# Performance work log

Measured on AMD Instinct MI355X. Metric: run time of the kernel, lower is better.

The kernel has to match this reference:

```python
import jax, jax.numpy as jnp
import numpy as np

B, L, D, H, PD = 1, 512, 1024, 16, 128
HW = D // H  # 64


def _layernorm(x, g, b, eps=1e-5):
    mu = jnp.mean(x, axis=-1, keepdims=True)
    var = jnp.var(x, axis=-1, keepdims=True)
    return (x - mu) * jax.lax.rsqrt(var + eps) * g + b


def setup_inputs() -> dict:
    key = jax.random.key(0)
    ks = jax.random.split(key, 16)
    s = 0.02
    return {
        "sequence_state": jax.random.normal(ks[0], (B, L, D), jnp.float32),
        "pairwise_state": jax.random.normal(ks[1], (B, L, L, PD), jnp.float32),
        "mask": jnp.ones((B, L), dtype=bool),
        # layernorm before attention
        "ln1_g": jnp.ones((D,), jnp.float32),
        "ln1_b": jnp.zeros((D,), jnp.float32),
        # attention params (weights stored [in, out])
        "proj_w": jax.random.normal(ks[2], (D, 3 * H * HW), jnp.float32) * s,
        "g_w": jax.random.normal(ks[3], (D, H * HW), jnp.float32) * s,
        "g_b": jnp.ones((H * HW,), jnp.float32),
        "o_w": jax.random.normal(ks[4], (H * HW, D), jnp.float32) * s,
        "o_b": jnp.zeros((D,), jnp.float32),
        # pair-to-sequence bias
        "p2s_ln_g": jnp.ones((PD,), jnp.float32),
        "p2s_ln_b": jnp.zeros((PD,), jnp.float32),
        "p2s_w": jax.random.normal(ks[5], (PD, H), jnp.float32) * s,
        # residue MLP
        "mlp_ln_g": jnp.ones((D,), jnp.float32),
        "mlp_ln_b": jnp.zeros((D,), jnp.float32),
        "mlp_w1": jax.random.normal(ks[6], (D, 4 * D), jnp.float32) * s,
        "mlp_b1": jnp.zeros((4 * D,), jnp.float32),
        "mlp_w2": jax.random.normal(ks[7], (4 * D, D), jnp.float32) * s,
        "mlp_b2": jnp.zeros((D,), jnp.float32),
    }


def reference(sequence_state, pairwise_state, mask,
              ln1_g, ln1_b, proj_w, g_w, g_b, o_w, o_b,
              p2s_ln_g, p2s_ln_b, p2s_w,
              mlp_ln_g, mlp_ln_b, mlp_w1, mlp_b1, mlp_w2, mlp_b2):
    # PairToSequence: LN over pairwise feature dim, then project to per-head bias
    z = _layernorm(pairwise_state, p2s_ln_g, p2s_ln_b)
    bias = jnp.einsum("bqkp,ph->bhqk", z, p2s_w)  # [B,H,L,L]

    # Pre-attention layernorm
    y = _layernorm(sequence_state, ln1_g, ln1_b)

    # Gated attention with pairwise bias
    t = (y @ proj_w).reshape(B, L, H, 3 * HW)
    q, k, v = jnp.split(t, 3, axis=-1)  # each [B,L,H,HW]
    q = q * (HW ** -0.5)
    a = jnp.einsum("bqhc,bkhc->bhqk", q, k) + bias
    a = jnp.where(mask[:, None, None, :], a, -jnp.inf)
    a = jax.nn.softmax(a, axis=-1)
    o = jnp.einsum("bhqk,bkhc->bqhc", a, v).reshape(B, L, H * HW)
    gate = jax.nn.sigmoid(y @ g_w + g_b)
    o = (gate * o) @ o_w + o_b

    # residual (dropout=0 -> identity)
    s = sequence_state + o

    # ResidueMLP: x + Linear(ReLU(Linear(LN(x))))
    h = _layernorm(s, mlp_ln_g, mlp_ln_b)
    h = jax.nn.relu(h @ mlp_w1 + mlp_b1) @ mlp_w2 + mlp_b2
    return s + h
```

## Files before the change

### kernel.cpp

```cpp
#include <hip/hip_runtime.h>


typedef __attribute__((ext_vector_type(8))) short bfrag;
typedef __attribute__((ext_vector_type(4))) float f32x4;
typedef unsigned short ushort_t;
typedef unsigned int u32;

#define AS1 __attribute__((address_space(1)))
#define AS3 __attribute__((address_space(3)))

__device__ __forceinline__ void gll16(const void* g, void* l) {
  __builtin_amdgcn_global_load_lds((const AS1 u32*)g, (AS3 u32*)l, 16, 0, 0);
}

__device__ __forceinline__ unsigned short f2b(float x) {
  union { float f; unsigned u; } a; a.f = x;
  unsigned r = a.u + 0x7fffu + ((a.u >> 16) & 1u);
  return (unsigned short)(r >> 16);
}
__device__ __forceinline__ unsigned pack2(float a, float b) {
  return (unsigned)f2b(a) | ((unsigned)f2b(b) << 16);
}

#define OFF_GW    ((size_t)0)
#define OFF_SB    ((size_t)65536)
#define OFF_P     (OFF_SB   + (size_t)16777216)
#define OFF_Y     (OFF_P    + (size_t)8388608)
#define OFF_QS    (OFF_Y    + (size_t)1048576)
#define OFF_KS    (OFF_QS   + (size_t)1048576)
#define OFF_VT    (OFF_KS   + (size_t)1048576)
#define OFF_GATE  (OFF_VT   + (size_t)1048576)
#define OFF_OG    (OFF_GATE + (size_t)2097152)
#define OFF_S     (OFF_OG   + (size_t)1048576)
#define OFF_HLN   (OFF_S    + (size_t)2097152)
#define OFF_H1    (OFF_HLN  + (size_t)1048576)
#define OFF_PART  (OFF_H1   + (size_t)4194304)
#define OFF_WPG   (OFF_PART + (size_t)8388608)
#define OFF_WO    (OFF_WPG  + (size_t)8388608)
#define OFF_W1    (OFF_WO   + (size_t)2097152)
#define OFF_W2    (OFF_W1   + (size_t)8388608)

__global__ __launch_bounds__(256) void p2s_setup(
    const float* __restrict__ g, const float* __restrict__ b,
    const float* __restrict__ w, float* __restrict__ gw) {
  int t = threadIdx.x;
  for (int i = t; i < 2048; i += 256) {
    int h = i >> 7, f = i & 127;
    gw[h * 128 + f] = g[f] * w[f * 16 + h];
  }
  if (t < 16) {
    float a = 0.f, c = 0.f;
    for (int f = 0; f < 128; f++) { a += g[f] * w[f * 16 + t]; c += b[f] * w[f * 16 + t]; }
    gw[2048 + t] = a;
    gw[2064 + t] = c;
  }
}

__global__ __launch_bounds__(256) void p2s_main(
    const float* __restrict__ pw, const float* __restrict__ gw,
    float* __restrict__ biasOut) {
  __shared__ float xs[16 * 132];
  __shared__ float gwt[16 * 132];
  const int t = threadIdx.x;
  const long pair0 = (long)blockIdx.x * 16;
  const int p = t >> 4;
  const int h = t & 15;
  const int f0 = h * 8;

  float4 w0 = *(const float4*)&gw[p * 128 + f0];
  float4 w1 = *(const float4*)&gw[p * 128 + f0 + 4];
  *(float4*)&gwt[p * 132 + f0]     = w0;
  *(float4*)&gwt[p * 132 + f0 + 4] = w1;
  const float* src = pw + pair0 * 128 + (long)t * 8;
  float4 x0 = *(const float4*)src;
  float4 x1 = *(const float4*)(src + 4);
  *(float4*)&xs[p * 132 + f0]     = x0;
  *(float4*)&xs[p * 132 + f0 + 4] = x1;

  float s  = x0.x + x0.y + x0.z + x0.w + x1.x + x1.y + x1.z + x1.w;
  float sq = x0.x*x0.x + x0.y*x0.y + x0.z*x0.z + x0.w*x0.w
           + x1.x*x1.x + x1.y*x1.y + x1.z*x1.z + x1.w*x1.w;
#pragma unroll
  for (int m = 1; m < 16; m <<= 1) { s += __shfl_xor(s, m); sq += __shfl_xor(sq, m); }
  float mu  = s * (1.f / 128.f);
  float var = sq * (1.f / 128.f) - mu * mu;
  float rs  = rsqrtf(var + 1e-5f);

  __syncthreads();

  float acc = 0.f;
#pragma unroll 8
  for (int f = 0; f < 128; f += 4) {
    float4 xv = *(const float4*)&xs[p * 132 + f];
    float4 wv = *(const float4*)&gwt[h * 132 + f];
    acc += xv.x * wv.x + xv.y * wv.y + xv.z * wv.z + xv.w * wv.w;
  }
  float c1 = gw[2048 + h], c2 = gw[2064 + h];
  biasOut[(long)h * 262144 + pair0 + p] = rs * (acc - mu * c1) + c2;
}

__device__ __forceinline__ void transp_tile(
    const float* __restrict__ W, ushort_t* __restrict__ Wt, int K, int N,
    int bx, int by, int tid) {
  __shared__ float tile[64][65];
  int n0 = bx * 64, k0 = by * 64;
  int tr = tid >> 4, tc = (tid & 15) * 4;
#pragma unroll
  for (int i = 0; i < 4; i++) {
    int r = tr + i * 16;
    float4 v = *(const float4*)&W[(long)(k0 + r) * N + n0 + tc];
    tile[r][tc] = v.x; tile[r][tc + 1] = v.y; tile[r][tc + 2] = v.z; tile[r][tc + 3] = v.w;
  }
  __syncthreads();
  int nr = tid >> 2, kk = (tid & 3) * 16;
  ushort_t* dst = Wt + (long)(n0 + nr) * K + k0 + kk;
  uint4 q;
  q.x = pack2(tile[kk + 0][nr], tile[kk + 1][nr]);
  q.y = pack2(tile[kk + 2][nr], tile[kk + 3][nr]);
  q.z = pack2(tile[kk + 4][nr], tile[kk + 5][nr]);
  q.w = pack2(tile[kk + 6][nr], tile[kk + 7][nr]);
  *(uint4*)dst = q;
  uint4 q2;
  q2.x = pack2(tile[kk + 8][nr],  tile[kk + 9][nr]);
  q2.y = pack2(tile[kk + 10][nr], tile[kk + 11][nr]);
  q2.z = pack2(tile[kk + 12][nr], tile[kk + 13][nr]);
  q2.w = pack2(tile[kk + 14][nr], tile[kk + 15][nr]);
  *(uint4*)(dst + 8) = q2;
}

__global__ __launch_bounds__(256) void transpose_all(
    const float* __restrict__ proj_w, const float* __restrict__ g_w,
    const float* __restrict__ o_w, const float* __restrict__ w1,
    const float* __restrict__ w2,
    ushort_t* __restrict__ wpg, ushort_t* __restrict__ wo,
    ushort_t* __restrict__ w1t, ushort_t* __restrict__ w2t) {
  int id = blockIdx.x, tid = threadIdx.x;
  if (id < 768)       transp_tile(proj_w, wpg, 1024, 3072, id % 48, id / 48, tid);
  else if (id < 1024) { int j = id - 768;  transp_tile(g_w, wpg + (long)3072 * 1024, 1024, 1024, j % 16, j / 16, tid); }
  else if (id < 1280) { int j = id - 1024; transp_tile(o_w, wo, 1024, 1024, j % 16, j / 16, tid); }
  else if (id < 2304) { int j = id - 1280; transp_tile(w1, w1t, 1024, 4096, j % 64, j / 64, tid); }
  else                { int j = id - 2304; transp_tile(w2, w2t, 4096, 1024, j % 16, j / 16, tid); }
}

__global__ __launch_bounds__(256) void ln_rows(
    const float* __restrict__ x, const float* __restrict__ g,
    const float* __restrict__ b, ushort_t* __restrict__ out) {
  __shared__ float ps[8];
  int row = blockIdx.x, t = threadIdx.x;
  float4 v = *(const float4*)(x + (long)row * 1024 + t * 4);
  float s  = v.x + v.y + v.z + v.w;
  float sq = v.x*v.x + v.y*v.y + v.z*v.z + v.w*v.w;
#pragma unroll
  for (int k = 1; k < 64; k <<= 1) { s += __shfl_xor(s, k); sq += __shfl_xor(sq, k); }
  if ((t & 63) == 0) { ps[t >> 6] = s; ps[4 + (t >> 6)] = sq; }
  __syncthreads();
  s  = ps[0] + ps[1] + ps[2] + ps[3];
  sq = ps[4] + ps[5] + ps[6] + ps[7];
  float mu = s * (1.f / 1024.f);
  float rs = rsqrtf(sq * (1.f / 1024.f) - mu * mu + 1e-5f);
  float4 gv = *(const float4*)(g + t * 4);
  float4 bv = *(const float4*)(b + t * 4);
  uint2 o;
  o.x = pack2((v.x - mu) * rs * gv.x + bv.x, (v.y - mu) * rs * gv.y + bv.y);
  o.y = pack2((v.z - mu) * rs * gv.z + bv.z, (v.w - mu) * rs * gv.w + bv.w);
  *(uint2*)(out + (long)row * 1024 + t * 4) = o;
}

template <int EPI>
__global__ __launch_bounds__(256) void gemm128(
    const ushort_t* __restrict__ A, const ushort_t* __restrict__ Bt,
    int lda, int ldb, int Ksplit,
    const float* __restrict__ bias1,
    float* __restrict__ outF, ushort_t* __restrict__ outH, int ldc,
    ushort_t* __restrict__ qs, ushort_t* __restrict__ ks,
    ushort_t* __restrict__ vt, float* __restrict__ gatebuf) {
  __shared__ ushort_t As[64 * 32];
  __shared__ ushort_t Bs[128 * 32];
  const int tid = threadIdx.x;
  const int w = tid >> 6, lane = tid & 63;
  const int ln = lane & 15, quad = lane >> 4;
  const int wm = w >> 1, wn = w & 1;
  const int m0 = blockIdx.y * 64, n0 = blockIdx.x * 128;
  const int z = blockIdx.z;
  const int Koff = (EPI == 0) ? z * Ksplit : 0;

  const ushort_t* ga  = A  + (long)(m0 + (tid >> 2)) * lda + Koff + (tid & 3) * 8;
  const ushort_t* gb0 = Bt + (long)(n0 + (tid >> 2)) * ldb + Koff + (tid & 3) * 8;
  const ushort_t* gb1 = gb0 + (long)64 * ldb;
  unsigned wofs = __builtin_amdgcn_readfirstlane(w * 1024);
  char* lA  = (char*)As + wofs;
  char* lB0 = (char*)Bs + wofs;
  char* lB1 = (char*)Bs + 4096 + wofs;

  f32x4 acc[2][4];
#pragma unroll
  for (int i = 0; i < 2; i++)
#pragma unroll
    for (int j = 0; j < 4; j++) acc[i][j] = (f32x4){0.f, 0.f, 0.f, 0.f};

  for (int k0 = 0; k0 < Ksplit; k0 += 32) {
    gll16(ga + k0, lA);
    gll16(gb0 + k0, lB0);
    gll16(gb1 + k0, lB1);
    __syncthreads();
    bfrag a0 = *(const bfrag*)&As[(wm * 32 + ln) * 32 + quad * 8];
    bfrag a1 = *(const bfrag*)&As[(wm * 32 + 16 + ln) * 32 + quad * 8];
#pragma unroll
    for (int bn = 0; bn < 4; bn++) {
      bfrag b = *(const bfrag*)&Bs[(wn * 64 + bn * 16 + ln) * 32 + quad * 8];
      acc[0][bn] = __builtin_amdgcn_mfma_f32_16x16x32_bf16(a0, b, acc[0][bn], 0, 0, 0);
      acc[1][bn] = __builtin_amdgcn_mfma_f32_16x16x32_bf16(a1, b, acc[1][bn], 0, 0, 0);
    }
    __syncthreads();
  }

#pragma unroll
  for (int am = 0; am < 2; am++) {
#pragma unroll
    for (int bn = 0; bn < 4; bn++) {
      int ocol = n0 + wn * 64 + bn * 16 + ln;
#pragma unroll
      for (int r = 0; r < 4; r++) {
        int orow = m0 + wm * 32 + am * 16 + quad * 4 + r;
        float v = acc[am][bn][r];
        if (EPI == 0) {
          outF[(long)z * 524288 + (long)orow * ldc + ocol] = v;
        } else if (EPI == 3) {
          v = fmaxf(v + bias1[ocol], 0.f);
          outH[(long)orow * ldc + ocol] = f2b(v);
        } else if (EPI == 6) {
          if (ocol < 3072) {
            int h = ocol / 192, j = ocol - h * 192;
            if (j < 64)       qs[((long)h * 512 + orow) * 64 + j] = f2b(v * 0.125f);
            else if (j < 128) ks[((long)h * 512 + orow) * 64 + (j - 64)] = f2b(v);
            else              vt[((long)h * 64 + (j - 128)) * 512 + orow] = f2b(v);
          } else {
            int gcol = ocol - 3072;
            float gv = v + bias1[gcol];
            gatebuf[(long)orow * 1024 + gcol] = 1.f / (1.f + __expf(-gv));
          }
        }
      }
    }
  }
}

template <int EPI>
__global__ __launch_bounds__(256) void gemm_bt(
    const ushort_t* __restrict__ A, const ushort_t* __restrict__ Bt,
    const float* __restrict__ bias2, int ldb2,
    float* __restrict__ outF, ushort_t* __restrict__ outH,
    int K, int ldc, long sAz, long sBz, long sCz, long sB2z) {
  __shared__ ushort_t As[64 * 40];
  __shared__ ushort_t Bs[64 * 40];
  const int tid = threadIdx.x;
  const int wave = tid >> 6, lane = tid & 63;
  const int srow = tid >> 2;
  const int skcol = (tid & 3) * 8;
  const int m0 = blockIdx.y * 64, n0 = blockIdx.x * 64;
  const int z = blockIdx.z;
  const ushort_t* Az = A + (long)z * sAz + (long)m0 * K;
  const ushort_t* Bz = Bt + (long)z * sBz + (long)n0 * K;
  const int ln = lane & 15, quad = lane >> 4;

  f32x4 acc[4];
#pragma unroll
  for (int i = 0; i < 4; i++) acc[i] = (f32x4){0.f, 0.f, 0.f, 0.f};

  for (int k0 = 0; k0 < K; k0 += 32) {
    uint4 av = *(const uint4*)(Az + (long)srow * K + k0 + skcol);
    uint4 bv = *(const uint4*)(Bz + (long)srow * K + k0 + skcol);
    __syncthreads();
    *(uint4*)&As[srow * 40 + skcol] = av;
    *(uint4*)&Bs[srow * 40 + skcol] = bv;
    __syncthreads();
    bfrag a = *(const bfrag*)&As[(wave * 16 + ln) * 40 + quad * 8];
#pragma unroll
    for (int t4 = 0; t4 < 4; t4++) {
      bfrag b = *(const bfrag*)&Bs[(t4 * 16 + ln) * 40 + quad * 8];
      acc[t4] = __builtin_amdgcn_mfma_f32_16x16x32_bf16(a, b, acc[t4], 0, 0, 0);
    }
  }

#pragma unroll
  for (int t4 = 0; t4 < 4; t4++) {
    int ocol = n0 + t4 * 16 + ln;
#pragma unroll
    for (int r = 0; r < 4; r++) {
      int orow = m0 + wave * 16 + quad * 4 + r;
      float v = acc[t4][r];
      long oidx = (long)z * sCz + (long)orow * ldc + ocol;
      if (EPI == 4) {
        v += bias2[(long)z * sB2z + (long)orow * ldb2 + ocol];
        outF[oidx] = v;
      } else {
        v *= bias2[(long)z * sB2z + (long)orow * ldb2 + ocol];
        outH[oidx] = f2b(v);
      }
    }
  }
}

__global__ __launch_bounds__(256) void softmax_rows(
    const float* __restrict__ S, ushort_t* __restrict__ P) {
  int row = blockIdx.x * 4 + (threadIdx.x >> 6);
  int lane = threadIdx.x & 63;
  const float* sr = S + (long)row * 512 + lane * 8;
  float4 a = *(const float4*)sr;
  float4 b = *(const float4*)(sr + 4);
  float m = fmaxf(fmaxf(fmaxf(a.x, a.y), fmaxf(a.z, a.w)),
                  fmaxf(fmaxf(b.x, b.y), fmaxf(b.z, b.w)));
#pragma unroll
  for (int k = 1; k < 64; k <<= 1) m = fmaxf(m, __shfl_xor(m, k));
  float e0 = __expf(a.x - m), e1 = __expf(a.y - m), e2 = __expf(a.z - m), e3 = __expf(a.w - m);
  float e4 = __expf(b.x - m), e5 = __expf(b.y - m), e6 = __expf(b.z - m), e7 = __expf(b.w - m);
  float s = e0 + e1 + e2 + e3 + e4 + e5 + e6 + e7;
#pragma unroll
  for (int k = 1; k < 64; k <<= 1) s += __shfl_xor(s, k);
  float inv = 1.f / s;
  uint4 o;
  o.x = pack2(e0 * inv, e1 * inv);
  o.y = pack2(e2 * inv, e3 * inv);
  o.z = pack2(e4 * inv, e5 * inv);
  o.w = pack2(e6 * inv, e7 * inv);
  *(uint4*)(P + (long)row * 512 + lane * 8) = o;
}

template <int DO_LN>
__global__ __launch_bounds__(256) void finalize_row(
    const float* __restrict__ resid, const float* __restrict__ part,
    const float* __restrict__ bias,
    const float* __restrict__ g, const float* __restrict__ b,
    float* __restrict__ s_out, ushort_t* __restrict__ h_out) {
  __shared__ float ps[8];
  int row = blockIdx.x, t = threadIdx.x;
  long base = (long)row * 1024 + t * 4;
  float4 v = *(const float4*)(resid + base);
#pragma unroll
  for (int zz = 0; zz < 4; zz++) {
    float4 p = *(const float4*)(part + (long)zz * 524288 + base);
    v.x += p.x; v.y += p.y; v.z += p.z; v.w += p.w;
  }
  float4 bv = *(const float4*)(bias + t * 4);
  v.x += bv.x; v.y += bv.y; v.z += bv.z; v.w += bv.w;
  *(float4*)(s_out + base) = v;
  if (DO_LN) {
    float s  = v.x + v.y + v.z + v.w;
    float sq = v.x*v.x + v.y*v.y + v.z*v.z + v.w*v.w;
#pragma unroll
    for (int k = 1; k < 64; k <<= 1) { s += __shfl_xor(s, k); sq += __shfl_xor(sq, k); }
    if ((t & 63) == 0) { ps[t >> 6] = s; ps[4 + (t >> 6)] = sq; }
    __syncthreads();
    s  = ps[0] + ps[1] + ps[2] + ps[3];
    sq = ps[4] + ps[5] + ps[6] + ps[7];
    float mu = s * (1.f / 1024.f);
    float rs = rsqrtf(sq * (1.f / 1024.f) - mu * mu + 1e-5f);
    float4 gv = *(const float4*)(g + t * 4);
    float4 bb = *(const float4*)(b + t * 4);
    uint2 o;
    o.x = pack2((v.x - mu) * rs * gv.x + bb.x, (v.y - mu) * rs * gv.y + bb.y);
    o.y = pack2((v.z - mu) * rs * gv.z + bb.z, (v.w - mu) * rs * gv.w + bb.w);
    *(uint2*)(h_out + base) = o;
  }
}

extern "C" void kernel_launch(void* const* d_in, const int* in_sizes, int n_in,
                              void* d_out, int out_size, void* d_ws, size_t ws_size,
                              hipStream_t stream) {
  const float* seq    = (const float*)d_in[0];
  const float* pw     = (const float*)d_in[1];
  const float* ln1_g  = (const float*)d_in[3];
  const float* ln1_b  = (const float*)d_in[4];
  const float* proj_w = (const float*)d_in[5];
  const float* g_w    = (const float*)d_in[6];
  const float* g_b    = (const float*)d_in[7];
  const float* o_w    = (const float*)d_in[8];
  const float* o_b    = (const float*)d_in[9];
  const float* p2s_g  = (const float*)d_in[10];
  const float* p2s_b  = (const float*)d_in[11];
  const float* p2s_w  = (const float*)d_in[12];
  const float* mlp_g  = (const float*)d_in[13];
  const float* mlp_bb = (const float*)d_in[14];
  const float* w1     = (const float*)d_in[15];
  const float* b1     = (const float*)d_in[16];
  const float* w2     = (const float*)d_in[17];
  const float* b2     = (const float*)d_in[18];
  float* out = (float*)d_out;
  char* ws = (char*)d_ws;

  float* gw          = (float*)(ws + OFF_GW);
  float* Sb          = (float*)(ws + OFF_SB);
  ushort_t* P        = (ushort_t*)(ws + OFF_P);
  ushort_t* ybf      = (ushort_t*)(ws + OFF_Y);
  ushort_t* qs       = (ushort_t*)(ws + OFF_QS);
  ushort_t* ks       = (ushort_t*)(ws + OFF_KS);
  ushort_t* vt       = (ushort_t*)(ws + OFF_VT);
  float* gatebuf     = (float*)(ws + OFF_GATE);
  ushort_t* og       = (ushort_t*)(ws + OFF_OG);
  float* sbuf        = (float*)(ws + OFF_S);
  ushort_t* hln      = (ushort_t*)(ws + OFF_HLN);
  ushort_t* h1       = (ushort_t*)(ws + OFF_H1);
  float* part        = (float*)(ws + OFF_PART);
  ushort_t* wpg      = (ushort_t*)(ws + OFF_WPG);
  ushort_t* wo       = (ushort_t*)(ws + OFF_WO);
  ushort_t* w1t      = (ushort_t*)(ws + OFF_W1);
  ushort_t* w2t      = (ushort_t*)(ws + OFF_W2);

  p2s_setup<<<1, 256, 0, stream>>>(p2s_g, p2s_b, p2s_w, gw);
  transpose_all<<<3328, 256, 0, stream>>>(proj_w, g_w, o_w, w1, w2, wpg, wo, w1t, w2t);
  p2s_main<<<16384, 256, 0, stream>>>(pw, gw, Sb);
  ln_rows<<<512, 256, 0, stream>>>(seq, ln1_g, ln1_b, ybf);

  gemm128<6><<<dim3(32, 8, 1), 256, 0, stream>>>(ybf, wpg, 1024, 1024, 1024,
                                                 g_b, nullptr, nullptr, 0,
                                                 qs, ks, vt, gatebuf);
  gemm_bt<4><<<dim3(8, 8, 16), 256, 0, stream>>>(qs, ks, Sb, 512, Sb, nullptr,
                                                 64, 512, 32768, 32768, 262144, 262144);
  softmax_rows<<<2048, 256, 0, stream>>>(Sb, P);
  gemm_bt<5><<<dim3(1, 8, 16), 256, 0, stream>>>(P, vt, gatebuf, 1024, nullptr, og,
                                                 512, 1024, 262144, 32768, 64, 64);
  gemm128<0><<<dim3(8, 8, 4), 256, 0, stream>>>(og, wo, 1024, 1024, 256,
                                                nullptr, part, nullptr, 1024,
                                                nullptr, nullptr, nullptr, nullptr);
  finalize_row<1><<<512, 256, 0, stream>>>(seq, part, o_b, mlp_g, mlp_bb, sbuf, hln);
  gemm128<3><<<dim3(32, 8, 1), 256, 0, stream>>>(hln, w1t, 1024, 1024, 1024,
                                                 b1, nullptr, h1, 4096,
                                                 nullptr, nullptr, nullptr, nullptr);
  gemm128<0><<<dim3(8, 8, 4), 256, 0, stream>>>(h1, w2t, 4096, 4096, 1024,
                                                nullptr, part, nullptr, 1024,
                                                nullptr, nullptr, nullptr, nullptr);
  finalize_row<0><<<512, 256, 0, stream>>>(sbuf, part, b2, nullptr, nullptr, out, nullptr);
}
```

Before: 377.5 us.

## Fuse preprocessing into one kernel, add flash attention, atomic split-K epilogues

Merges the p2s bias, weight transposes and first layernorm into a single kernel, and stores the pair bias as bf16 instead of fp32. Replaces the QK^T GEMM, softmax and PV GEMM with one fused flash-attention kernel that applies the bias and gate, so the fp32 score matrix and the probability buffer are never materialised. Split-K GEMMs now atomicAdd straight into the residual buffers, which removes the partial buffers and the finalize passes. In exchange it relies on atomic float accumulation, whose order is nondeterministic, and it lowers the precision of the bias.

Result: slower. 428.4 us (+13.5%).

```diff
diff --git a/kernel.cpp b/kernel.cpp
--- a/kernel.cpp
+++ b/kernel.cpp
@@ -21,11 +21,12 @@
 __device__ __forceinline__ unsigned pack2(float a, float b) {
   return (unsigned)f2b(a) | ((unsigned)f2b(b) << 16);
 }
-
-#define OFF_GW    ((size_t)0)
-#define OFF_SB    ((size_t)65536)
-#define OFF_P     (OFF_SB   + (size_t)16777216)
-#define OFF_Y     (OFF_P    + (size_t)8388608)
+__device__ __forceinline__ float b2f(ushort_t u) {
+  union { float f; unsigned v; } a; a.v = ((unsigned)u) << 16; return a.f;
+}
+
+#define OFF_BIASH ((size_t)0)
+#define OFF_Y     ((size_t)8388608)
 #define OFF_QS    (OFF_Y    + (size_t)1048576)
 #define OFF_KS    (OFF_QS   + (size_t)1048576)
 #define OFF_VT    (OFF_KS   + (size_t)1048576)
@@ -34,75 +35,15 @@
 #define OFF_S     (OFF_OG   + (size_t)1048576)
 #define OFF_HLN   (OFF_S    + (size_t)2097152)
 #define OFF_H1    (OFF_HLN  + (size_t)1048576)
-#define OFF_PART  (OFF_H1   + (size_t)4194304)
-#define OFF_WPG   (OFF_PART + (size_t)8388608)
+#define OFF_WPG   (OFF_H1   + (size_t)4194304)
 #define OFF_WO    (OFF_WPG  + (size_t)8388608)
 #define OFF_W1    (OFF_WO   + (size_t)2097152)
 #define OFF_W2    (OFF_W1   + (size_t)8388608)
 
-__global__ __launch_bounds__(256) void p2s_setup(
-    const float* __restrict__ g, const float* __restrict__ b,
-    const float* __restrict__ w, float* __restrict__ gw) {
-  int t = threadIdx.x;
-  for (int i = t; i < 2048; i += 256) {
-    int h = i >> 7, f = i & 127;
-    gw[h * 128 + f] = g[f] * w[f * 16 + h];
-  }
-  if (t < 16) {
-    float a = 0.f, c = 0.f;
-    for (int f = 0; f < 128; f++) { a += g[f] * w[f * 16 + t]; c += b[f] * w[f * 16 + t]; }
-    gw[2048 + t] = a;
-    gw[2064 + t] = c;
-  }
-}
-
-__global__ __launch_bounds__(256) void p2s_main(
-    const float* __restrict__ pw, const float* __restrict__ gw,
-    float* __restrict__ biasOut) {
-  __shared__ float xs[16 * 132];
-  __shared__ float gwt[16 * 132];
-  const int t = threadIdx.x;
-  const long pair0 = (long)blockIdx.x * 16;
-  const int p = t >> 4;
-  const int h = t & 15;
-  const int f0 = h * 8;
-
-  float4 w0 = *(const float4*)&gw[p * 128 + f0];
-  float4 w1 = *(const float4*)&gw[p * 128 + f0 + 4];
-  *(float4*)&gwt[p * 132 + f0]     = w0;
-  *(float4*)&gwt[p * 132 + f0 + 4] = w1;
-  const float* src = pw + pair0 * 128 + (long)t * 8;
-  float4 x0 = *(const float4*)src;
-  float4 x1 = *(const float4*)(src + 4);
-  *(float4*)&xs[p * 132 + f0]     = x0;
-  *(float4*)&xs[p * 132 + f0 + 4] = x1;
-
-  float s  = x0.x + x0.y + x0.z + x0.w + x1.x + x1.y + x1.z + x1.w;
-  float sq = x0.x*x0.x + x0.y*x0.y + x0.z*x0.z + x0.w*x0.w
-           + x1.x*x1.x + x1.y*x1.y + x1.z*x1.z + x1.w*x1.w;
-#pragma unroll
-  for (int m = 1; m < 16; m <<= 1) { s += __shfl_xor(s, m); sq += __shfl_xor(sq, m); }
-  float mu  = s * (1.f / 128.f);
-  float var = sq * (1.f / 128.f) - mu * mu;
-  float rs  = rsqrtf(var + 1e-5f);
-
-  __syncthreads();
-
-  float acc = 0.f;
-#pragma unroll 8
-  for (int f = 0; f < 128; f += 4) {
-    float4 xv = *(const float4*)&xs[p * 132 + f];
-    float4 wv = *(const float4*)&gwt[h * 132 + f];
-    acc += xv.x * wv.x + xv.y * wv.y + xv.z * wv.z + xv.w * wv.w;
-  }
-  float c1 = gw[2048 + h], c2 = gw[2064 + h];
-  biasOut[(long)h * 262144 + pair0 + p] = rs * (acc - mu * c1) + c2;
-}
-
 __device__ __forceinline__ void transp_tile(
     const float* __restrict__ W, ushort_t* __restrict__ Wt, int K, int N,
-    int bx, int by, int tid) {
-  __shared__ float tile[64][65];
+    int bx, int by, int tid, float* smem) {
+  float (*tile)[65] = (float(*)[65])smem;
   int n0 = bx * 64, k0 = by * 64;
   int tr = tid >> 4, tc = (tid & 15) * 4;
 #pragma unroll
@@ -128,42 +69,103 @@
   *(uint4*)(dst + 8) = q2;
 }
 
-__global__ __launch_bounds__(256) void transpose_all(
+__global__ __launch_bounds__(256) void mega1(
+    const float* __restrict__ pw,
+    const float* __restrict__ p2s_g, const float* __restrict__ p2s_b,
+    const float* __restrict__ p2s_w,
     const float* __restrict__ proj_w, const float* __restrict__ g_w,
     const float* __restrict__ o_w, const float* __restrict__ w1,
     const float* __restrict__ w2,
-    ushort_t* __restrict__ wpg, ushort_t* __restrict__ wo,
-    ushort_t* __restrict__ w1t, ushort_t* __restrict__ w2t) {
-  int id = blockIdx.x, tid = threadIdx.x;
-  if (id < 768)       transp_tile(proj_w, wpg, 1024, 3072, id % 48, id / 48, tid);
-  else if (id < 1024) { int j = id - 768;  transp_tile(g_w, wpg + (long)3072 * 1024, 1024, 1024, j % 16, j / 16, tid); }
-  else if (id < 1280) { int j = id - 1024; transp_tile(o_w, wo, 1024, 1024, j % 16, j / 16, tid); }
-  else if (id < 2304) { int j = id - 1280; transp_tile(w1, w1t, 1024, 4096, j % 64, j / 64, tid); }
-  else                { int j = id - 2304; transp_tile(w2, w2t, 4096, 1024, j % 16, j / 16, tid); }
-}
-
-__global__ __launch_bounds__(256) void ln_rows(
-    const float* __restrict__ x, const float* __restrict__ g,
-    const float* __restrict__ b, ushort_t* __restrict__ out) {
-  __shared__ float ps[8];
-  int row = blockIdx.x, t = threadIdx.x;
-  float4 v = *(const float4*)(x + (long)row * 1024 + t * 4);
-  float s  = v.x + v.y + v.z + v.w;
-  float sq = v.x*v.x + v.y*v.y + v.z*v.z + v.w*v.w;
-#pragma unroll
-  for (int k = 1; k < 64; k <<= 1) { s += __shfl_xor(s, k); sq += __shfl_xor(sq, k); }
-  if ((t & 63) == 0) { ps[t >> 6] = s; ps[4 + (t >> 6)] = sq; }
-  __syncthreads();
-  s  = ps[0] + ps[1] + ps[2] + ps[3];
-  sq = ps[4] + ps[5] + ps[6] + ps[7];
-  float mu = s * (1.f / 1024.f);
-  float rs = rsqrtf(sq * (1.f / 1024.f) - mu * mu + 1e-5f);
-  float4 gv = *(const float4*)(g + t * 4);
-  float4 bv = *(const float4*)(b + t * 4);
-  uint2 o;
-  o.x = pack2((v.x - mu) * rs * gv.x + bv.x, (v.y - mu) * rs * gv.y + bv.y);
-  o.y = pack2((v.z - mu) * rs * gv.z + bv.z, (v.w - mu) * rs * gv.w + bv.w);
-  *(uint2*)(out + (long)row * 1024 + t * 4) = o;
+    const float* __restrict__ seq, const float* __restrict__ ln1_g,
+    const float* __restrict__ ln1_b, const float* __restrict__ o_b,
+    ushort_t* __restrict__ biasH, ushort_t* __restrict__ wpg,
+    ushort_t* __restrict__ wo, ushort_t* __restrict__ w1t,
+    ushort_t* __restrict__ w2t, ushort_t* __restrict__ ybf,
+    float* __restrict__ sbuf) {
+  __shared__ float smem[4528];
+  const int id = blockIdx.x, t = threadIdx.x;
+
+  if (id < 16384) {
+    float* gwt = smem;
+    float* xs  = smem + 2112;
+    float* cc  = smem + 4224;
+    float* res = smem + 4256;
+
+#pragma unroll
+    for (int i = t; i < 2048; i += 256) {
+      int h = i >> 7, f = i & 127;
+      gwt[h * 132 + f] = p2s_g[f] * p2s_w[f * 16 + h];
+    }
+    if (t < 32) {
+      int h = t & 15;
+      const float* src = (t >> 4) ? p2s_b : p2s_g;
+      float sum = 0.f;
+      for (int f = 0; f < 128; f++) sum += src[f] * p2s_w[f * 16 + h];
+      cc[t] = sum;
+    }
+
+    const long pair0 = (long)id * 16;
+    const int p = t >> 4, h = t & 15, f0 = h * 8;
+    const float* src = pw + pair0 * 128 + (long)t * 8;
+    float4 x0 = *(const float4*)src;
+    float4 x1 = *(const float4*)(src + 4);
+    *(float4*)&xs[p * 132 + f0]     = x0;
+    *(float4*)&xs[p * 132 + f0 + 4] = x1;
+
+    float s  = x0.x + x0.y + x0.z + x0.w + x1.x + x1.y + x1.z + x1.w;
+    float sq = x0.x*x0.x + x0.y*x0.y + x0.z*x0.z + x0.w*x0.w
+             + x1.x*x1.x + x1.y*x1.y + x1.z*x1.z + x1.w*x1.w;
+#pragma unroll
+    for (int m = 1; m < 16; m <<= 1) { s += __shfl_xor(s, m); sq += __shfl_xor(sq, m); }
+    float mu  = s * (1.f / 128.f);
+    float var = sq * (1.f / 128.f) - mu * mu;
+    float rs  = rsqrtf(var + 1e-5f);
+
+    __syncthreads();
+
+    float acc = 0.f;
+#pragma unroll 8
+    for (int f = 0; f < 128; f += 4) {
+      float4 xv = *(const float4*)&xs[p * 132 + f];
+      float4 wv = *(const float4*)&gwt[h * 132 + f];
+      acc += xv.x * wv.x + xv.y * wv.y + xv.z * wv.z + xv.w * wv.w;
+    }
+    float val = rs * (acc - mu * cc[h]) + cc[16 + h];
+    res[h * 17 + p] = val;
+    __syncthreads();
+    int h2 = t >> 4, p2 = t & 15;
+    biasH[(long)h2 * 262144 + pair0 + p2] = f2b(res[h2 * 17 + p2]);
+  } else if (id < 19712) {
+    int j = id - 16384;
+    if (j < 768)       transp_tile(proj_w, wpg, 1024, 3072, j % 48, j / 48, t, smem);
+    else if (j < 1024) { j -= 768;  transp_tile(g_w, wpg + (long)3072 * 1024, 1024, 1024, j % 16, j / 16, t, smem); }
+    else if (j < 1280) { j -= 1024; transp_tile(o_w, wo, 1024, 1024, j % 16, j / 16, t, smem); }
+    else if (j < 2304) { j -= 1280; transp_tile(w1, w1t, 1024, 4096, j % 64, j / 64, t, smem); }
+    else               { j -= 2304; transp_tile(w2, w2t, 4096, 1024, j % 16, j / 16, t, smem); }
+  } else {
+    int row = id - 19712;
+    long base = (long)row * 1024 + t * 4;
+    float4 v = *(const float4*)(seq + base);
+    float4 ob = *(const float4*)(o_b + t * 4);
+    float4 sv; sv.x = v.x + ob.x; sv.y = v.y + ob.y; sv.z = v.z + ob.z; sv.w = v.w + ob.w;
+    *(float4*)(sbuf + base) = sv;
+    float s  = v.x + v.y + v.z + v.w;
+    float sq = v.x*v.x + v.y*v.y + v.z*v.z + v.w*v.w;
+#pragma unroll
+    for (int k = 1; k < 64; k <<= 1) { s += __shfl_xor(s, k); sq += __shfl_xor(sq, k); }
+    if ((t & 63) == 0) { smem[t >> 6] = s; smem[4 + (t >> 6)] = sq; }
+    __syncthreads();
+    s  = smem[0] + smem[1] + smem[2] + smem[3];
+    sq = smem[4] + smem[5] + smem[6] + smem[7];
+    float mu = s * (1.f / 1024.f);
+    float rsd = rsqrtf(sq * (1.f / 1024.f) - mu * mu + 1e-5f);
+    float4 gv = *(const float4*)(ln1_g + t * 4);
+    float4 bv = *(const float4*)(ln1_b + t * 4);
+    uint2 o;
+    o.x = pack2((v.x - mu) * rsd * gv.x + bv.x, (v.y - mu) * rsd * gv.y + bv.y);
+    o.y = pack2((v.z - mu) * rsd * gv.z + bv.z, (v.w - mu) * rsd * gv.w + bv.w);
+    *(uint2*)(ybf + base) = o;
+  }
 }
 
 template <int EPI>
@@ -182,7 +184,7 @@
   const int wm = w >> 1, wn = w & 1;
   const int m0 = blockIdx.y * 64, n0 = blockIdx.x * 128;
   const int z = blockIdx.z;
-  const int Koff = (EPI == 0) ? z * Ksplit : 0;
+  const int Koff = (EPI == 7) ? z * Ksplit : 0;
 
   const ushort_t* ga  = A  + (long)(m0 + (tid >> 2)) * lda + Koff + (tid & 3) * 8;
   const ushort_t* gb0 = Bt + (long)(n0 + (tid >> 2)) * ldb + Koff + (tid & 3) * 8;
@@ -223,9 +225,7 @@
       for (int r = 0; r < 4; r++) {
         int orow = m0 + wm * 32 + am * 16 + quad * 4 + r;
         float v = acc[am][bn][r];
-        if (EPI == 0) {
-          outF[(long)z * 524288 + (long)orow * ldc + ocol] = v;
-        } else if (EPI == 3) {
+        if (EPI == 3) {
           v = fmaxf(v + bias1[ocol], 0.f);
           outH[(long)orow * ldc + ocol] = f2b(v);
         } else if (EPI == 6) {
@@ -239,129 +239,160 @@
             float gv = v + bias1[gcol];
             gatebuf[(long)orow * 1024 + gcol] = 1.f / (1.f + __expf(-gv));
           }
+        } else {
+          atomicAdd(&outF[(long)orow * ldc + ocol], v);
         }
       }
     }
   }
 }
 
-template <int EPI>
-__global__ __launch_bounds__(256) void gemm_bt(
-    const ushort_t* __restrict__ A, const ushort_t* __restrict__ Bt,
-    const float* __restrict__ bias2, int ldb2,
-    float* __restrict__ outF, ushort_t* __restrict__ outH,
-    int K, int ldc, long sAz, long sBz, long sCz, long sB2z) {
-  __shared__ ushort_t As[64 * 40];
-  __shared__ ushort_t Bs[64 * 40];
+__global__ __launch_bounds__(256) void flash_attn(
+    const ushort_t* __restrict__ qs, const ushort_t* __restrict__ ks,
+    const ushort_t* __restrict__ vt, const ushort_t* __restrict__ biasH,
+    const float* __restrict__ gate, ushort_t* __restrict__ og) {
+  __shared__ ushort_t Qs[64 * 72];
+  __shared__ ushort_t Ks[64 * 72];
+  __shared__ ushort_t Vs[64 * 72];
+  __shared__ ushort_t Ps[64 * 72];
   const int tid = threadIdx.x;
-  const int wave = tid >> 6, lane = tid & 63;
-  const int srow = tid >> 2;
-  const int skcol = (tid & 3) * 8;
-  const int m0 = blockIdx.y * 64, n0 = blockIdx.x * 64;
-  const int z = blockIdx.z;
-  const ushort_t* Az = A + (long)z * sAz + (long)m0 * K;
-  const ushort_t* Bz = Bt + (long)z * sBz + (long)n0 * K;
-  const int ln = lane & 15, quad = lane >> 4;
-
-  f32x4 acc[4];
-#pragma unroll
-  for (int i = 0; i < 4; i++) acc[i] = (f32x4){0.f, 0.f, 0.f, 0.f};
-
-  for (int k0 = 0; k0 < K; k0 += 32) {
-    uint4 av = *(const uint4*)(Az + (long)srow * K + k0 + skcol);
-    uint4 bv = *(const uint4*)(Bz + (long)srow * K + k0 + skcol);
-    __syncthreads();
-    *(uint4*)&As[srow * 40 + skcol] = av;
-    *(uint4*)&Bs[srow * 40 + skcol] = bv;
-    __syncthreads();
-    bfrag a = *(const bfrag*)&As[(wave * 16 + ln) * 40 + quad * 8];
-#pragma unroll
-    for (int t4 = 0; t4 < 4; t4++) {
-      bfrag b = *(const bfrag*)&Bs[(t4 * 16 + ln) * 40 + quad * 8];
-      acc[t4] = __builtin_amdgcn_mfma_f32_16x16x32_bf16(a, b, acc[t4], 0, 0, 0);
-    }
-  }
-
+  const int w = tid >> 6, lane = tid & 63, ln = lane & 15, quad = lane >> 4;
+  const int h = blockIdx.x, q0 = blockIdx.y * 64;
+  const int r = tid >> 2, c0 = (tid & 3) * 16;
+
+  { const ushort_t* src = qs + ((long)(h * 512 + q0 + r)) * 64 + c0;
+    *(uint4*)&Qs[r * 72 + c0]     = *(const uint4*)src;
+    *(uint4*)&Qs[r * 72 + c0 + 8] = *(const uint4*)(src + 8); }
+
+  float m_[4], l_[4];
+  f32x4 Oacc[4];
+#pragma unroll
+  for (int i = 0; i < 4; i++) { m_[i] = -1e30f; l_[i] = 0.f; Oacc[i] = (f32x4){0.f,0.f,0.f,0.f}; }
+
+  for (int kt = 0; kt < 8; kt++) {
+    const int k0 = kt * 64;
+    __syncthreads();
+    { const ushort_t* srcK = ks + ((long)(h * 512 + k0 + r)) * 64 + c0;
+      *(uint4*)&Ks[r * 72 + c0]     = *(const uint4*)srcK;
+      *(uint4*)&Ks[r * 72 + c0 + 8] = *(const uint4*)(srcK + 8);
+      const ushort_t* srcV = vt + ((long)(h * 64 + r)) * 512 + k0 + c0;
+      *(uint4*)&Vs[r * 72 + c0]     = *(const uint4*)srcV;
+      *(uint4*)&Vs[r * 72 + c0 + 8] = *(const uint4*)(srcV + 8); }
+
+    f32x4 acc[4];
+    const ushort_t* bp = biasH + ((long)h * 512 + q0 + w * 16 + quad * 4) * 512 + k0 + ln;
+#pragma unroll
+    for (int t4 = 0; t4 < 4; t4++)
+#pragma unroll
+      for (int rr = 0; rr < 4; rr++)
+        acc[t4][rr] = b2f(bp[(long)rr * 512 + t4 * 16]);
+
+    __syncthreads();
+#pragma unroll
+    for (int s = 0; s < 2; s++) {
+      bfrag a = *(const bfrag*)&Qs[(w * 16 + ln) * 72 + s * 32 + quad * 8];
+#pragma unroll
+      for (int t4 = 0; t4 < 4; t4++) {
+        bfrag b = *(const bfrag*)&Ks[(t4 * 16 + ln) * 72 + s * 32 + quad * 8];
+        acc[t4] = __builtin_amdgcn_mfma_f32_16x16x32_bf16(a, b, acc[t4], 0, 0, 0);
+      }
+    }
+
+    float mt[4];
+#pragma unroll
+    for (int rr = 0; rr < 4; rr++)
+      mt[rr] = fmaxf(fmaxf(acc[0][rr], acc[1][rr]), fmaxf(acc[2][rr], acc[3][rr]));
+#pragma unroll
+    for (int xm = 1; xm < 16; xm <<= 1)
+#pragma unroll
+      for (int rr = 0; rr < 4; rr++) mt[rr] = fmaxf(mt[rr], __shfl_xor(mt[rr], xm));
+    float al[4];
+#pragma unroll
+    for (int rr = 0; rr < 4; rr++) {
+      float mn = fmaxf(m_[rr], mt[rr]);
+      al[rr] = __expf(m_[rr] - mn);
+      m_[rr] = mn;
+    }
+#pragma unroll
+    for (int t4 = 0; t4 < 4; t4++)
+#pragma unroll
+      for (int rr = 0; rr < 4; rr++)
+        acc[t4][rr] = __expf(acc[t4][rr] - m_[rr]);
+    float rs[4];
+#pragma unroll
+    for (int rr = 0; rr < 4; rr++)
+      rs[rr] = acc[0][rr] + acc[1][rr] + acc[2][rr] + acc[3][rr];
+#pragma unroll
+    for (int xm = 1; xm < 16; xm <<= 1)
+#pragma unroll
+      for (int rr = 0; rr < 4; rr++) rs[rr] += __shfl_xor(rs[rr], xm);
+#pragma unroll
+    for (int rr = 0; rr < 4; rr++) l_[rr] = l_[rr] * al[rr] + rs[rr];
+#pragma unroll
+    for (int t4 = 0; t4 < 4; t4++)
+#pragma unroll
+      for (int rr = 0; rr < 4; rr++) Oacc[t4][rr] *= al[rr];
+
+#pragma unroll
+    for (int t4 = 0; t4 < 4; t4++)
+#pragma unroll
+      for (int rr = 0; rr < 4; rr++)
+        Ps[(w * 16 + quad * 4 + rr) * 72 + t4 * 16 + ln] = f2b(acc[t4][rr]);
+    __syncthreads();
+
+#pragma unroll
+    for (int s = 0; s < 2; s++) {
+      bfrag a = *(const bfrag*)&Ps[(w * 16 + ln) * 72 + s * 32 + quad * 8];
+#pragma unroll
+      for (int t4 = 0; t4 < 4; t4++) {
+        bfrag b = *(const bfrag*)&Vs[(t4 * 16 + ln) * 72 + s * 32 + quad * 8];
+        Oacc[t4] = __builtin_amdgcn_mfma_f32_16x16x32_bf16(a, b, Oacc[t4], 0, 0, 0);
+      }
+    }
+  }
+
+  float inv[4];
+#pragma unroll
+  for (int rr = 0; rr < 4; rr++) inv[rr] = 1.f / l_[rr];
 #pragma unroll
   for (int t4 = 0; t4 < 4; t4++) {
-    int ocol = n0 + t4 * 16 + ln;
-#pragma unroll
-    for (int r = 0; r < 4; r++) {
-      int orow = m0 + wave * 16 + quad * 4 + r;
-      float v = acc[t4][r];
-      long oidx = (long)z * sCz + (long)orow * ldc + ocol;
-      if (EPI == 4) {
-        v += bias2[(long)z * sB2z + (long)orow * ldb2 + ocol];
-        outF[oidx] = v;
-      } else {
-        v *= bias2[(long)z * sB2z + (long)orow * ldb2 + ocol];
-        outH[oidx] = f2b(v);
-      }
-    }
-  }
-}
-
-__global__ __launch_bounds__(256) void softmax_rows(
-    const float* __restrict__ S, ushort_t* __restrict__ P) {
-  int row = blockIdx.x * 4 + (threadIdx.x >> 6);
-  int lane = threadIdx.x & 63;
-  const float* sr = S + (long)row * 512 + lane * 8;
-  float4 a = *(const float4*)sr;
-  float4 b = *(const float4*)(sr + 4);
-  float m = fmaxf(fmaxf(fmaxf(a.x, a.y), fmaxf(a.z, a.w)),
-                  fmaxf(fmaxf(b.x, b.y), fmaxf(b.z, b.w)));
-#pragma unroll
-  for (int k = 1; k < 64; k <<= 1) m = fmaxf(m, __shfl_xor(m, k));
-  float e0 = __expf(a.x - m), e1 = __expf(a.y - m), e2 = __expf(a.z - m), e3 = __expf(a.w - m);
-  float e4 = __expf(b.x - m), e5 = __expf(b.y - m), e6 = __expf(b.z - m), e7 = __expf(b.w - m);
-  float s = e0 + e1 + e2 + e3 + e4 + e5 + e6 + e7;
-#pragma unroll
-  for (int k = 1; k < 64; k <<= 1) s += __shfl_xor(s, k);
-  float inv = 1.f / s;
-  uint4 o;
-  o.x = pack2(e0 * inv, e1 * inv);
-  o.y = pack2(e2 * inv, e3 * inv);
-  o.z = pack2(e4 * inv, e5 * inv);
-  o.w = pack2(e6 * inv, e7 * inv);
-  *(uint4*)(P + (long)row * 512 + lane * 8) = o;
-}
-
-template <int DO_LN>
-__global__ __launch_bounds__(256) void finalize_row(
-    const float* __restrict__ resid, const float* __restrict__ part,
-    const float* __restrict__ bias,
-    const float* __restrict__ g, const float* __restrict__ b,
-    float* __restrict__ s_out, ushort_t* __restrict__ h_out) {
+#pragma unroll
+    for (int rr = 0; rr < 4; rr++) {
+      int grow = q0 + w * 16 + quad * 4 + rr;
+      int gcol = h * 64 + t4 * 16 + ln;
+      float gt = gate[(long)grow * 1024 + gcol];
+      og[(long)grow * 1024 + gcol] = f2b(Oacc[t4][rr] * inv[rr] * gt);
+    }
+  }
+}
+
+__global__ __launch_bounds__(256) void ln2(
+    const float* __restrict__ sbuf, const float* __restrict__ g,
+    const float* __restrict__ b, const float* __restrict__ b2,
+    ushort_t* __restrict__ hln, float* __restrict__ out) {
   __shared__ float ps[8];
   int row = blockIdx.x, t = threadIdx.x;
   long base = (long)row * 1024 + t * 4;
-  float4 v = *(const float4*)(resid + base);
-#pragma unroll
-  for (int zz = 0; zz < 4; zz++) {
-    float4 p = *(const float4*)(part + (long)zz * 524288 + base);
-    v.x += p.x; v.y += p.y; v.z += p.z; v.w += p.w;
-  }
-  float4 bv = *(const float4*)(bias + t * 4);
-  v.x += bv.x; v.y += bv.y; v.z += bv.z; v.w += bv.w;
-  *(float4*)(s_out + base) = v;
-  if (DO_LN) {
-    float s  = v.x + v.y + v.z + v.w;
-    float sq = v.x*v.x + v.y*v.y + v.z*v.z + v.w*v.w;
-#pragma unroll
-    for (int k = 1; k < 64; k <<= 1) { s += __shfl_xor(s, k); sq += __shfl_xor(sq, k); }
-    if ((t & 63) == 0) { ps[t >> 6] = s; ps[4 + (t >> 6)] = sq; }
-    __syncthreads();
-    s  = ps[0] + ps[1] + ps[2] + ps[3];
-    sq = ps[4] + ps[5] + ps[6] + ps[7];
-    float mu = s * (1.f / 1024.f);
-    float rs = rsqrtf(sq * (1.f / 1024.f) - mu * mu + 1e-5f);
-    float4 gv = *(const float4*)(g + t * 4);
-    float4 bb = *(const float4*)(b + t * 4);
-    uint2 o;
-    o.x = pack2((v.x - mu) * rs * gv.x + bb.x, (v.y - mu) * rs * gv.y + bb.y);
-    o.y = pack2((v.z - mu) * rs * gv.z + bb.z, (v.w - mu) * rs * gv.w + bb.w);
-    *(uint2*)(h_out + base) = o;
-  }
+  float4 v = *(const float4*)(sbuf + base);
+  float4 b2v = *(const float4*)(b2 + t * 4);
+  float4 ov; ov.x = v.x + b2v.x; ov.y = v.y + b2v.y; ov.z = v.z + b2v.z; ov.w = v.w + b2v.w;
+  *(float4*)(out + base) = ov;
+  float s  = v.x + v.y + v.z + v.w;
+  float sq = v.x*v.x + v.y*v.y + v.z*v.z + v.w*v.w;
+#pragma unroll
+  for (int k = 1; k < 64; k <<= 1) { s += __shfl_xor(s, k); sq += __shfl_xor(sq, k); }
+  if ((t & 63) == 0) { ps[t >> 6] = s; ps[4 + (t >> 6)] = sq; }
+  __syncthreads();
+  s  = ps[0] + ps[1] + ps[2] + ps[3];
+  sq = ps[4] + ps[5] + ps[6] + ps[7];
+  float mu = s * (1.f / 1024.f);
+  float rsd = rsqrtf(sq * (1.f / 1024.f) - mu * mu + 1e-5f);
+  float4 gv = *(const float4*)(g + t * 4);
+  float4 bv = *(const float4*)(b + t * 4);
+  uint2 o;
+  o.x = pack2((v.x - mu) * rsd * gv.x + bv.x, (v.y - mu) * rsd * gv.y + bv.y);
+  o.y = pack2((v.z - mu) * rsd * gv.z + bv.z, (v.w - mu) * rsd * gv.w + bv.w);
+  *(uint2*)(hln + base) = o;
 }
 
 extern "C" void kernel_launch(void* const* d_in, const int* in_sizes, int n_in,
@@ -388,46 +419,37 @@
   float* out = (float*)d_out;
   char* ws = (char*)d_ws;
 
-  float* gw          = (float*)(ws + OFF_GW);
-  float* Sb          = (float*)(ws + OFF_SB);
-  ushort_t* P        = (ushort_t*)(ws + OFF_P);
-  ushort_t* ybf      = (ushort_t*)(ws + OFF_Y);
-  ushort_t* qs       = (ushort_t*)(ws + OFF_QS);
-  ushort_t* ks       = (ushort_t*)(ws + OFF_KS);
-  ushort_t* vt       = (ushort_t*)(ws + OFF_VT);
-  float* gatebuf     = (float*)(ws + OFF_GATE);
-  ushort_t* og       = (ushort_t*)(ws + OFF_OG);
-  float* sbuf        = (float*)(ws + OFF_S);
-  ushort_t* hln      = (ushort_t*)(ws + OFF_HLN);
-  ushort_t* h1       = (ushort_t*)(ws + OFF_H1);
-  float* part        = (float*)(ws + OFF_PART);
-  ushort_t* wpg      = (ushort_t*)(ws + OFF_WPG);
-  ushort_t* wo       = (ushort_t*)(ws + OFF_WO);
-  ushort_t* w1t      = (ushort_t*)(ws + OFF_W1);
-  ushort_t* w2t      = (ushort_t*)(ws + OFF_W2);
-
-  p2s_setup<<<1, 256, 0, stream>>>(p2s_g, p2s_b, p2s_w, gw);
-  transpose_all<<<3328, 256, 0, stream>>>(proj_w, g_w, o_w, w1, w2, wpg, wo, w1t, w2t);
-  p2s_main<<<16384, 256, 0, stream>>>(pw, gw, Sb);
-  ln_rows<<<512, 256, 0, stream>>>(seq, ln1_g, ln1_b, ybf);
-
+  ushort_t* biasH = (ushort_t*)(ws + OFF_BIASH);
+  ushort_t* ybf   = (ushort_t*)(ws + OFF_Y);
+  ushort_t* qs    = (ushort_t*)(ws + OFF_QS);
+  ushort_t* ks    = (ushort_t*)(ws + OFF_KS);
+  ushort_t* vt    = (ushort_t*)(ws + OFF_VT);
+  float* gatebuf  = (float*)(ws + OFF_GATE);
+  ushort_t* og    = (ushort_t*)(ws + OFF_OG);
+  float* sbuf     = (float*)(ws + OFF_S);
+  ushort_t* hln   = (ushort_t*)(ws + OFF_HLN);
+  ushort_t* h1    = (ushort_t*)(ws + OFF_H1);
+  ushort_t* wpg   = (ushort_t*)(ws + OFF_WPG);
+  ushort_t* wo    = (ushort_t*)(ws + OFF_WO);
+  ushort_t* w1t   = (ushort_t*)(ws + OFF_W1);
+  ushort_t* w2t   = (ushort_t*)(ws + OFF_W2);
+
+  mega1<<<20224, 256, 0, stream>>>(pw, p2s_g, p2s_b, p2s_w,
+                                   proj_w, g_w, o_w, w1, w2,
+                                   seq, ln1_g, ln1_b, o_b,
+                                   biasH, wpg, wo, w1t, w2t, ybf, sbuf);
   gemm128<6><<<dim3(32, 8, 1), 256, 0, stream>>>(ybf, wpg, 1024, 1024, 1024,
                                                  g_b, nullptr, nullptr, 0,
                                                  qs, ks, vt, gatebuf);
-  gemm_bt<4><<<dim3(8, 8, 16), 256, 0, stream>>>(qs, ks, Sb, 512, Sb, nullptr,
-                                                 64, 512, 32768, 32768, 262144, 262144);
-  softmax_rows<<<2048, 256, 0, stream>>>(Sb, P);
-  gemm_bt<5><<<dim3(1, 8, 16), 256, 0, stream>>>(P, vt, gatebuf, 1024, nullptr, og,
-                                                 512, 1024, 262144, 32768, 64, 64);
-  gemm128<0><<<dim3(8, 8, 4), 256, 0, stream>>>(og, wo, 1024, 1024, 256,
-                                                nullptr, part, nullptr, 1024,
+  flash_attn<<<dim3(16, 8), 256, 0, stream>>>(qs, ks, vt, biasH, gatebuf, og);
+  gemm128<7><<<dim3(8, 8, 4), 256, 0, stream>>>(og, wo, 1024, 1024, 256,
+                                                nullptr, sbuf, nullptr, 1024,
                                                 nullptr, nullptr, nullptr, nullptr);
-  finalize_row<1><<<512, 256, 0, stream>>>(seq, part, o_b, mlp_g, mlp_bb, sbuf, hln);
+  ln2<<<512, 256, 0, stream>>>(sbuf, mlp_g, mlp_bb, b2, hln, out);
   gemm128<3><<<dim3(32, 8, 1), 256, 0, stream>>>(hln, w1t, 1024, 1024, 1024,
                                                  b1, nullptr, h1, 4096,
                                                  nullptr, nullptr, nullptr, nullptr);
-  gemm128<0><<<dim3(8, 8, 4), 256, 0, stream>>>(h1, w2t, 4096, 4096, 1024,
-                                                nullptr, part, nullptr, 1024,
+  gemm128<7><<<dim3(8, 8, 4), 256, 0, stream>>>(h1, w2t, 4096, 4096, 1024,
+                                                nullptr, out, nullptr, 1024,
                                                 nullptr, nullptr, nullptr, nullptr);
-  finalize_row<0><<<512, 256, 0, stream>>>(sbuf, part, b2, nullptr, nullptr, out, nullptr);
-}
+}
```
